# Performance work log

Hardware: AMD Instinct MI355X
Metric: run time of the kernel (lower is better)

## Reference

```python
import jax, jax.numpy as jnp
import numpy as np

N = 50000
E = 800000
F_IN = 512
HID = 32
HEADS = 8
CLS = 64
NEG_SLOPE = 0.2
EPS = 1e-16  # PyG softmax denominator epsilon


def setup_inputs() -> dict:
    key = jax.random.key(0)
    ks = jax.random.split(key, 10)
    x = jax.random.normal(ks[0], (N, F_IN), dtype=jnp.float32)
    edge_index = jax.random.randint(ks[1], (2, E), 0, N, dtype=jnp.int64)
    # layer 1: in=F_IN, heads=HEADS, out_per_head=HID, concat
    s1 = 1.0 / np.sqrt(F_IN)
    W1 = jax.random.normal(ks[2], (F_IN, HEADS * HID), dtype=jnp.float32) * s1
    att_src1 = jax.random.normal(ks[3], (HEADS, HID), dtype=jnp.float32) * 0.1
    att_dst1 = jax.random.normal(ks[4], (HEADS, HID), dtype=jnp.float32) * 0.1
    b1 = jnp.zeros((HEADS * HID,), dtype=jnp.float32)
    # layer 2: in=HEADS*HID, heads=1, out=CLS, no concat
    s2 = 1.0 / np.sqrt(HEADS * HID)
    W2 = jax.random.normal(ks[5], (HEADS * HID, CLS), dtype=jnp.float32) * s2
    att_src2 = jax.random.normal(ks[6], (1, CLS), dtype=jnp.float32) * 0.1
    att_dst2 = jax.random.normal(ks[7], (1, CLS), dtype=jnp.float32) * 0.1
    b2 = jnp.zeros((CLS,), dtype=jnp.float32)
    return {"x": x, "edge_index": edge_index,
            "W1": W1, "att_src1": att_src1, "att_dst1": att_dst1, "b1": b1,
            "W2": W2, "att_src2": att_src2, "att_dst2": att_dst2, "b2": b2}


def gat_conv(x, edge_index, W, att_src, att_dst, bias, concat):
    n = x.shape[0]
    heads, c = att_src.shape
    h = (x @ W).reshape(n, heads, c)                       # [N,H,C]
    # add self loops (PyG GATConv default)
    loop = jnp.arange(n, dtype=edge_index.dtype)
    src = jnp.concatenate([edge_index[0], loop])
    dst = jnp.concatenate([edge_index[1], loop])
    a_src = jnp.einsum('nhc,hc->nh', h, att_src)           # [N,H]
    a_dst = jnp.einsum('nhc,hc->nh', h, att_dst)
    e = a_src[src] + a_dst[dst]                            # [E',H]
    e = jax.nn.leaky_relu(e, NEG_SLOPE)
    # segment softmax over destination node
    m = jax.ops.segment_max(e, dst, num_segments=n)
    e = jnp.exp(e - jax.lax.stop_gradient(m)[dst])
    s = jax.ops.segment_sum(e, dst, num_segments=n)
    alpha = e / (s[dst] + EPS)                             # [E',H]
    msg = h[src] * alpha[:, :, None]                       # [E',H,C]
    out = jax.ops.segment_sum(msg, dst, num_segments=n)    # [N,H,C]
    out = out.reshape(n, heads * c) if concat else out.mean(axis=1)
    return out + bias


def reference(x, edge_index, W1, att_src1, att_dst1, b1, W2, att_src2, att_dst2, b2):
    h = gat_conv(x, edge_index, W1, att_src1, att_dst1, b1, concat=True)
    h = jax.nn.relu(h)
    # F.dropout with training=False (eval) is identity
    h = gat_conv(h, edge_index, W2, att_src2, att_dst2, b2, concat=False)
    return jax.nn.log_softmax(h, axis=1)
```

## Files before the change

kernel.cpp:

```cpp
#include <hip/hip_runtime.h>
#include <hip/hip_bf16.h>
#include <stdint.h>

#define F_IN 512
#define HID 32
#define HEADS 8
#define C1 (HEADS*HID)
#define CLS 64
#define NEG 0.2f
#define EPS 1e-16f

typedef __bf16 bf16x8 __attribute__((ext_vector_type(8)));
typedef __bf16 bf16x4 __attribute__((ext_vector_type(4)));
typedef float  f32x4  __attribute__((ext_vector_type(4)));

__device__ __forceinline__ float leaky(float v) { return v > 0.f ? v : NEG * v; }

__global__ __launch_bounds__(256) void cvt_x(const float* __restrict__ x,
    __bf16* __restrict__ xb, int total8) {
  int i = blockIdx.x * 256 + threadIdx.x;
  if (i >= total8) return;
  const float4* p = (const float4*)(x + (size_t)i * 8);
  float4 a = p[0], b = p[1];
  bf16x8 o;
  o[0] = (__bf16)a.x; o[1] = (__bf16)a.y; o[2] = (__bf16)a.z; o[3] = (__bf16)a.w;
  o[4] = (__bf16)b.x; o[5] = (__bf16)b.y; o[6] = (__bf16)b.z; o[7] = (__bf16)b.w;
  *(bf16x8*)(xb + (size_t)i * 8) = o;
}

__global__ __launch_bounds__(256) void cvt_w1t(const float* __restrict__ W1,
    __bf16* __restrict__ w1t) {
  int i = blockIdx.x * 256 + threadIdx.x;
  int o0 = i * 8;
  int c = o0 >> 9, k0 = o0 & 511;
  bf16x8 o;
#pragma unroll
  for (int j = 0; j < 8; j++) o[j] = (__bf16)W1[(size_t)(k0 + j) * C1 + c];
  *(bf16x8*)(w1t + (size_t)o0) = o;
}

__global__ __launch_bounds__(256) void cvt_w2t(const float* __restrict__ W2,
    __bf16* __restrict__ w2t) {
  int i = blockIdx.x * 256 + threadIdx.x;
  if (i >= CLS * C1 / 8) return;
  int o0 = i * 8;
  int c = o0 >> 8, k0 = o0 & 255;
  bf16x8 o;
#pragma unroll
  for (int j = 0; j < 8; j++) o[j] = (__bf16)W2[(size_t)(k0 + j) * CLS + c];
  *(bf16x8*)(w2t + (size_t)o0) = o;
}

__global__ __launch_bounds__(256) void gemm1_mfma(const __bf16* __restrict__ A,
    const __bf16* __restrict__ Bt, __bf16* __restrict__ C, int M) {
  __shared__ __bf16 Al[128 * 32];
  __shared__ __bf16 Bl[128 * 32];
  const int tid  = threadIdx.x;
  const int lane = tid & 63;
  const int wave = tid >> 6;
  const int lm = lane & 15, q = lane >> 4;
  const int wr = (wave >> 1) * 64, wc = (wave & 1) * 64;
  const int bm = blockIdx.y * 128, bn = blockIdx.x * 128;

  const int srow = tid >> 2;
  const int skc  = (tid & 3) * 8;

  f32x4 acc[4][4];
#pragma unroll
  for (int i = 0; i < 4; i++)
#pragma unroll
    for (int j = 0; j < 4; j++) acc[i][j] = (f32x4){0.f, 0.f, 0.f, 0.f};

  const int ra0 = min(bm + srow, M - 1);
  const int ra1 = min(bm + srow + 64, M - 1);
  const int rb0 = bn + srow, rb1 = bn + srow + 64;

  bf16x8 va0, va1, vb0, vb1;
  va0 = *(const bf16x8*)(A + (size_t)ra0 * 512 + skc);
  va1 = *(const bf16x8*)(A + (size_t)ra1 * 512 + skc);
  vb0 = *(const bf16x8*)(Bt + (size_t)rb0 * 512 + skc);
  vb1 = *(const bf16x8*)(Bt + (size_t)rb1 * 512 + skc);

  for (int kk = 0; kk < 16; kk++) {
    __syncthreads();
    *(bf16x8*)(Al + srow * 32 + skc)        = va0;
    *(bf16x8*)(Al + (srow + 64) * 32 + skc) = va1;
    *(bf16x8*)(Bl + srow * 32 + skc)        = vb0;
    *(bf16x8*)(Bl + (srow + 64) * 32 + skc) = vb1;
    __syncthreads();
    if (kk + 1 < 16) {
      const int k0 = (kk + 1) * 32;
      va0 = *(const bf16x8*)(A + (size_t)ra0 * 512 + k0 + skc);
      va1 = *(const bf16x8*)(A + (size_t)ra1 * 512 + k0 + skc);
      vb0 = *(const bf16x8*)(Bt + (size_t)rb0 * 512 + k0 + skc);
      vb1 = *(const bf16x8*)(Bt + (size_t)rb1 * 512 + k0 + skc);
    }
    bf16x8 af[4], bfr[4];
#pragma unroll
    for (int mi = 0; mi < 4; mi++)
      af[mi] = *(const bf16x8*)(Al + (wr + mi * 16 + lm) * 32 + q * 8);
#pragma unroll
    for (int ni = 0; ni < 4; ni++)
      bfr[ni] = *(const bf16x8*)(Bl + (wc + ni * 16 + lm) * 32 + q * 8);
#pragma unroll
    for (int mi = 0; mi < 4; mi++)
#pragma unroll
      for (int ni = 0; ni < 4; ni++)
        acc[mi][ni] = __builtin_amdgcn_mfma_f32_16x16x32_bf16(af[mi], bfr[ni], acc[mi][ni], 0, 0, 0);
  }

#pragma unroll
  for (int mi = 0; mi < 4; mi++) {
#pragma unroll
    for (int ni = 0; ni < 4; ni++) {
      const int col = bn + wc + ni * 16 + lm;
#pragma unroll
      for (int r = 0; r < 4; r++) {
        const int row = bm + wr + mi * 16 + q * 4 + r;
        if (row < M) C[(size_t)row * C1 + col] = (__bf16)acc[mi][ni][r];
      }
    }
  }
}

__global__ __launch_bounds__(256) void gemm2_mfma(const __bf16* __restrict__ A,
    const __bf16* __restrict__ Bt, __bf16* __restrict__ C, int M) {
  __shared__ __bf16 Al[128 * 32];
  __shared__ __bf16 Bl[64 * 32];
  const int tid  = threadIdx.x;
  const int lane = tid & 63;
  const int wave = tid >> 6;
  const int lm = lane & 15, q = lane >> 4;
  const int wr = (wave >> 1) * 64, wc = (wave & 1) * 32;
  const int bm = blockIdx.x * 128;

  const int srow = tid >> 2;
  const int skc  = (tid & 3) * 8;

  f32x4 acc[4][2];
#pragma unroll
  for (int i = 0; i < 4; i++)
#pragma unroll
    for (int j = 0; j < 2; j++) acc[i][j] = (f32x4){0.f, 0.f, 0.f, 0.f};

  const int ra0 = min(bm + srow, M - 1);
  const int ra1 = min(bm + srow + 64, M - 1);

  bf16x8 va0, va1, vb;
  va0 = *(const bf16x8*)(A + (size_t)ra0 * C1 + skc);
  va1 = *(const bf16x8*)(A + (size_t)ra1 * C1 + skc);
  vb  = *(const bf16x8*)(Bt + (size_t)srow * C1 + skc);

  for (int kk = 0; kk < 8; kk++) {
    __syncthreads();
    *(bf16x8*)(Al + srow * 32 + skc)        = va0;
    *(bf16x8*)(Al + (srow + 64) * 32 + skc) = va1;
    *(bf16x8*)(Bl + srow * 32 + skc)        = vb;
    __syncthreads();
    if (kk + 1 < 8) {
      const int k0 = (kk + 1) * 32;
      va0 = *(const bf16x8*)(A + (size_t)ra0 * C1 + k0 + skc);
      va1 = *(const bf16x8*)(A + (size_t)ra1 * C1 + k0 + skc);
      vb  = *(const bf16x8*)(Bt + (size_t)srow * C1 + k0 + skc);
    }
    bf16x8 af[4], bfr[2];
#pragma unroll
    for (int mi = 0; mi < 4; mi++)
      af[mi] = *(const bf16x8*)(Al + (wr + mi * 16 + lm) * 32 + q * 8);
#pragma unroll
    for (int ni = 0; ni < 2; ni++)
      bfr[ni] = *(const bf16x8*)(Bl + (wc + ni * 16 + lm) * 32 + q * 8);
#pragma unroll
    for (int mi = 0; mi < 4; mi++)
#pragma unroll
      for (int ni = 0; ni < 2; ni++)
        acc[mi][ni] = __builtin_amdgcn_mfma_f32_16x16x32_bf16(af[mi], bfr[ni], acc[mi][ni], 0, 0, 0);
  }

#pragma unroll
  for (int mi = 0; mi < 4; mi++) {
#pragma unroll
    for (int ni = 0; ni < 2; ni++) {
      const int col = wc + ni * 16 + lm;
#pragma unroll
      for (int r = 0; r < 4; r++) {
        const int row = bm + wr + mi * 16 + q * 4 + r;
        if (row < M) C[(size_t)row * CLS + col] = (__bf16)acc[mi][ni][r];
      }
    }
  }
}

__global__ __launch_bounds__(256) void att_scores1(const __bf16* __restrict__ h1,
    const float* __restrict__ asw, const float* __restrict__ adw,
    float* __restrict__ a_src, float* __restrict__ a_dst, int N) {
  const int t = threadIdx.x, lane = t & 63;
  const int n = blockIdx.x * 4 + (t >> 6);
  if (n >= N) return;
  bf16x4 x = *(const bf16x4*)(h1 + (size_t)n * C1 + lane * 4);
  const float4 wsv = *(const float4*)(asw + lane * 4);
  const float4 wdv = *(const float4*)(adw + lane * 4);
  float ps = (float)x[0] * wsv.x + (float)x[1] * wsv.y + (float)x[2] * wsv.z + (float)x[3] * wsv.w;
  float pd = (float)x[0] * wdv.x + (float)x[1] * wdv.y + (float)x[2] * wdv.z + (float)x[3] * wdv.w;
#pragma unroll
  for (int o = 1; o <= 4; o <<= 1) { ps += __shfl_xor(ps, o); pd += __shfl_xor(pd, o); }
  if ((lane & 7) == 0) {
    a_src[(size_t)n * 8 + (lane >> 3)] = ps;
    a_dst[(size_t)n * 8 + (lane >> 3)] = pd;
  }
}

__global__ __launch_bounds__(256) void att_scores2(const __bf16* __restrict__ h2b,
    const float* __restrict__ asw, const float* __restrict__ adw,
    float* __restrict__ a_src, float* __restrict__ a_dst, int N) {
  const int t = threadIdx.x, lane = t & 63;
  const int n = blockIdx.x * 4 + (t >> 6);
  if (n >= N) return;
  float v  = (float)h2b[(size_t)n * CLS + lane];
  float ps = v * asw[lane];
  float pd = v * adw[lane];
#pragma unroll
  for (int o = 1; o < 64; o <<= 1) { ps += __shfl_xor(ps, o); pd += __shfl_xor(pd, o); }
  if (lane == 0) { a_src[n] = ps; a_dst[n] = pd; }
}

__global__ __launch_bounds__(256) void count_deg(const int* __restrict__ ei,
    int* __restrict__ deg, int E) {
  int e = blockIdx.x * 256 + threadIdx.x;
  if (e < E) atomicAdd(&deg[ei[E + e]], 1);
}

__global__ __launch_bounds__(1024) void scan_rows(const int* __restrict__ deg,
    int* __restrict__ rowstart, int N) {
  __shared__ int wpart[16];
  __shared__ int s_carry;
  const int t = threadIdx.x, lane = t & 63, wid = t >> 6;
  if (t == 0) s_carry = 0;
  __syncthreads();
  for (int base = 0; base < N; base += 8192) {
    int i0 = base + t * 8;
    int d0[8], s8 = 0;
#pragma unroll
    for (int k = 0; k < 8; k++) { int i = i0 + k; d0[k] = (i < N) ? deg[i] : 0; s8 += d0[k]; }
    int v = s8;
#pragma unroll
    for (int off = 1; off < 64; off <<= 1) { int x = __shfl_up(v, off); if (lane >= off) v += x; }
    if (lane == 63) wpart[wid] = v;
    __syncthreads();
    if (wid == 0) {
      int w = (lane < 16) ? wpart[lane] : 0;
#pragma unroll
      for (int off = 1; off < 16; off <<= 1) { int x = __shfl_up(w, off); if (lane >= off) w += x; }
      if (lane < 16) wpart[lane] = w;
    }
    __syncthreads();
    int excl = s_carry + (wid > 0 ? wpart[wid - 1] : 0) + v - s8;
#pragma unroll
    for (int k = 0; k < 8; k++) { int i = i0 + k; if (i < N) rowstart[i] = excl; excl += d0[k]; }
    __syncthreads();
    if (t == 0) s_carry += wpart[15];
    __syncthreads();
  }
  if (t == 0) rowstart[N] = s_carry;
}

__global__ __launch_bounds__(256) void scatter_csr(const int* __restrict__ ei,
    int* __restrict__ cur, int* __restrict__ csr_src, int E) {
  int e = blockIdx.x * 256 + threadIdx.x;
  if (e >= E) return;
  int s = ei[e], d = ei[E + e];
  int pos = atomicAdd(&cur[d], 1);
  csr_src[pos] = s;
}

__global__ __launch_bounds__(256) void gather1(const int* __restrict__ rowstart,
    const int* __restrict__ csr_src, const __bf16* __restrict__ h1,
    const float* __restrict__ as1, const float* __restrict__ ad1,
    const float* __restrict__ b1, __bf16* __restrict__ o1, int N) {
  const int t = threadIdx.x;
  const int d = blockIdx.x * 4 + (t >> 6);
  if (d >= N) return;
  const int lane = t & 63;
  const int e8 = lane >> 3, hh = lane & 7;
  const int r0 = rowstart[d];
  const int deg = rowstart[d + 1] - r0;

  const float addh = ad1[(size_t)d * 8 + hh];
  const float self_sc = leaky(as1[(size_t)d * 8 + hh] + addh);

  int   se[8];
  float sc[8];
#pragma unroll
  for (int ch = 0; ch < 8; ch++) {
    const int j = ch * 8 + e8;
    se[ch] = 0; sc[ch] = -3.4e38f;
    if (j < deg) {
      int s = csr_src[r0 + j];
      se[ch] = s;
      sc[ch] = leaky(as1[(size_t)s * 8 + hh] + addh);
    }
  }
  float mx = -3.4e38f;
#pragma unroll
  for (int ch = 0; ch < 8; ch++) mx = fmaxf(mx, sc[ch]);
  for (int j0 = 64; j0 < deg; j0 += 8) {
    int j = j0 + e8;
    if (j < deg) {
      int s = csr_src[r0 + j];
      mx = fmaxf(mx, leaky(as1[(size_t)s * 8 + hh] + addh));
    }
  }
  mx = fmaxf(mx, __shfl_xor(mx, 8));
  mx = fmaxf(mx, __shfl_xor(mx, 16));
  mx = fmaxf(mx, __shfl_xor(mx, 32));
  mx = fmaxf(mx, self_sc);

  float sum = 0.f;
#pragma unroll
  for (int ch = 0; ch < 8; ch++)
    if (ch * 8 + e8 < deg) sum += __expf(sc[ch] - mx);
  for (int j0 = 64; j0 < deg; j0 += 8) {
    int j = j0 + e8;
    if (j < deg) {
      int s = csr_src[r0 + j];
      sum += __expf(leaky(as1[(size_t)s * 8 + hh] + addh) - mx);
    }
  }
  sum += __shfl_xor(sum, 8);
  sum += __shfl_xor(sum, 16);
  sum += __shfl_xor(sum, 32);
  sum += __expf(self_sc - mx);
  const float inv = 1.f / (sum + EPS);

  float al[8];
#pragma unroll
  for (int ch = 0; ch < 8; ch++) al[ch] = __expf(sc[ch] - mx) * inv;
  const float al_self_byhh = __expf(self_sc - mx) * inv;

  const int p = lane >> 5, g = lane & 31, hg = g >> 2;
  float acc[8];
#pragma unroll
  for (int i = 0; i < 8; i++) acc[i] = 0.f;

#pragma unroll
  for (int it = 0; it < 32; it++) {
    if (it * 2 < deg) {
      const int   j   = it * 2 + p;
      const int   s_j = __shfl(se[it >> 2], (j & 7) * 8);
      const float a_j = __shfl(al[it >> 2], (j & 7) * 8 + hg);
      bf16x8 x = *(const bf16x8*)(h1 + (size_t)s_j * C1 + g * 8);
#pragma unroll
      for (int i = 0; i < 8; i++) acc[i] += a_j * (float)x[i];
    }
  }
  for (int j0 = 64; j0 < deg; j0 += 8) {
    int j = j0 + e8;
    int se2 = 0; float al2 = 0.f;
    if (j < deg) { se2 = csr_src[r0 + j]; al2 = __expf(leaky(as1[(size_t)se2 * 8 + hh] + addh) - mx) * inv; }
#pragma unroll
    for (int it = 0; it < 4; it++) {
      if (j0 + it * 2 < deg) {
        const int   jj  = it * 2 + p;
        const int   s_j = __shfl(se2, jj * 8);
        const float a_j = __shfl(al2, jj * 8 + hg);
        bf16x8 x = *(const bf16x8*)(h1 + (size_t)s_j * C1 + g * 8);
#pragma unroll
        for (int i = 0; i < 8; i++) acc[i] += a_j * (float)x[i];
      }
    }
  }
#pragma unroll
  for (int i = 0; i < 8; i++) acc[i] += __shfl_xor(acc[i], 32);

  const float a_selfh = __shfl(al_self_byhh, hg);
  if (lane < 32) {
    bf16x8 xs = *(const bf16x8*)(h1 + (size_t)d * C1 + g * 8);
    const float4 b4a = *(const float4*)(b1 + g * 8);
    const float4 b4b = *(const float4*)(b1 + g * 8 + 4);
    bf16x8 o;
    o[0] = (__bf16)fmaxf(acc[0] + a_selfh * (float)xs[0] + b4a.x, 0.f);
    o[1] = (__bf16)fmaxf(acc[1] + a_selfh * (float)xs[1] + b4a.y, 0.f);
    o[2] = (__bf16)fmaxf(acc[2] + a_selfh * (float)xs[2] + b4a.z, 0.f);
    o[3] = (__bf16)fmaxf(acc[3] + a_selfh * (float)xs[3] + b4a.w, 0.f);
    o[4] = (__bf16)fmaxf(acc[4] + a_selfh * (float)xs[4] + b4b.x, 0.f);
    o[5] = (__bf16)fmaxf(acc[5] + a_selfh * (float)xs[5] + b4b.y, 0.f);
    o[6] = (__bf16)fmaxf(acc[6] + a_selfh * (float)xs[6] + b4b.z, 0.f);
    o[7] = (__bf16)fmaxf(acc[7] + a_selfh * (float)xs[7] + b4b.w, 0.f);
    *(bf16x8*)(o1 + (size_t)d * C1 + g * 8) = o;
  }
}

__global__ __launch_bounds__(256) void gather2(const int* __restrict__ rowstart,
    const int* __restrict__ csr_src, const __bf16* __restrict__ h2b,
    const float* __restrict__ as2, const float* __restrict__ ad2,
    float* __restrict__ out, int N) {
  const int t = threadIdx.x, lane = t & 63;
  const int d = blockIdx.x * 4 + (t >> 6);
  if (d >= N) return;
  const int r0 = rowstart[d], deg = rowstart[d + 1] - r0;
  const float addd = ad2[d];
  const float self_sc = leaky(as2[d] + addd);

  int se = 0; float sc = -3.4e38f;
  if (lane < deg) { se = csr_src[r0 + lane]; sc = leaky(as2[se] + addd); }
  float mx = sc;
  for (int j0 = 64; j0 < deg; j0 += 64) {
    int j = j0 + lane;
    if (j < deg) mx = fmaxf(mx, leaky(as2[csr_src[r0 + j]] + addd));
  }
#pragma unroll
  for (int o = 1; o < 64; o <<= 1) mx = fmaxf(mx, __shfl_xor(mx, o));
  mx = fmaxf(mx, self_sc);

  float ex = (lane < deg) ? __expf(sc - mx) : 0.f;
  float sum = ex;
  for (int j0 = 64; j0 < deg; j0 += 64) {
    int j = j0 + lane;
    if (j < deg) sum += __expf(leaky(as2[csr_src[r0 + j]] + addd) - mx);
  }
#pragma unroll
  for (int o = 1; o < 64; o <<= 1) sum += __shfl_xor(sum, o);
  const float e_self = __expf(self_sc - mx);
  sum += e_self;
  const float inv = 1.f / (sum + EPS);
  const float alpha = ex * inv;
  const float al_self = e_self * inv;

  const int e8 = lane >> 3, c8 = lane & 7;
  float acc[8];
#pragma unroll
  for (int i = 0; i < 8; i++) acc[i] = 0.f;

#pragma unroll
  for (int it = 0; it < 8; it++) {
    if (it * 8 < deg) {
      const int   j   = it * 8 + e8;
      const int   s_j = __shfl(se, j);
      const float a_j = __shfl(alpha, j);
      bf16x8 x = *(const bf16x8*)(h2b + (size_t)s_j * CLS + c8 * 8);
#pragma unroll
      for (int i = 0; i < 8; i++) acc[i] += a_j * (float)x[i];
    }
  }
  for (int j0 = 64; j0 < deg; j0 += 64) {
    int j = j0 + lane;
    int se2 = 0; float al2 = 0.f;
    if (j < deg) { se2 = csr_src[r0 + j]; al2 = __expf(leaky(as2[se2] + addd) - mx) * inv; }
#pragma unroll
    for (int it = 0; it < 8; it++) {
      if (j0 + it * 8 < deg) {
        const int   jj  = it * 8 + e8;
        const int   s_j = __shfl(se2, jj);
        const float a_j = __shfl(al2, jj);
        bf16x8 x = *(const bf16x8*)(h2b + (size_t)s_j * CLS + c8 * 8);
#pragma unroll
        for (int i = 0; i < 8; i++) acc[i] += a_j * (float)x[i];
      }
    }
  }
#pragma unroll
  for (int i = 0; i < 8; i++) {
    acc[i] += __shfl_xor(acc[i], 8);
    acc[i] += __shfl_xor(acc[i], 16);
    acc[i] += __shfl_xor(acc[i], 32);
  }
  if (lane < 8) {
    bf16x8 xs = *(const bf16x8*)(h2b + (size_t)d * CLS + c8 * 8);
    float4 o0, o1v;
    o0.x  = acc[0] + al_self * (float)xs[0];
    o0.y  = acc[1] + al_self * (float)xs[1];
    o0.z  = acc[2] + al_self * (float)xs[2];
    o0.w  = acc[3] + al_self * (float)xs[3];
    o1v.x = acc[4] + al_self * (float)xs[4];
    o1v.y = acc[5] + al_self * (float)xs[5];
    o1v.z = acc[6] + al_self * (float)xs[6];
    o1v.w = acc[7] + al_self * (float)xs[7];
    *(float4*)(out + (size_t)d * CLS + c8 * 8)     = o0;
    *(float4*)(out + (size_t)d * CLS + c8 * 8 + 4) = o1v;
  }
}

__global__ __launch_bounds__(256) void final_lsm(float* __restrict__ out,
    const float* __restrict__ b2, int N) {
  const int t = threadIdx.x, c = t & 63;
  const int n = blockIdx.x * 4 + (t >> 6);
  if (n >= N) return;
  float v = out[(size_t)n * CLS + c] + b2[c];
  float mx = v;
#pragma unroll
  for (int o = 1; o < 64; o <<= 1) mx = fmaxf(mx, __shfl_xor(mx, o));
  float ex = __expf(v - mx);
  float sm = ex;
#pragma unroll
  for (int o = 1; o < 64; o <<= 1) sm += __shfl_xor(sm, o);
  out[(size_t)n * CLS + c] = v - mx - __logf(sm);
}

extern "C" void kernel_launch(void* const* d_in, const int* in_sizes, int n_in,
                              void* d_out, int out_size, void* d_ws, size_t ws_size,
                              hipStream_t stream) {
  const float* x        = (const float*)d_in[0];
  const int*   ei       = (const int*)d_in[1];
  const float* W1       = (const float*)d_in[2];
  const float* att_src1 = (const float*)d_in[3];
  const float* att_dst1 = (const float*)d_in[4];
  const float* b1       = (const float*)d_in[5];
  const float* W2       = (const float*)d_in[6];
  const float* att_src2 = (const float*)d_in[7];
  const float* att_dst2 = (const float*)d_in[8];
  const float* b2       = (const float*)d_in[9];
  float* out = (float*)d_out;

  const int N  = in_sizes[0] / F_IN;
  const int E  = in_sizes[1] / 2;

  char* ws = (char*)d_ws;
  size_t off = 0;
  auto alloc = [&](size_t bytes) -> void* {
    void* p = ws + off;
    off += (bytes + 255) & ~(size_t)255;
    return p;
  };
  __bf16* h1  = (__bf16*)alloc((size_t)N * C1 * 2);
  __bf16* o1  = (__bf16*)alloc((size_t)N * C1 * 2);
  float*  as1 = (float*)alloc((size_t)N * HEADS * 4);
  float*  ad1 = (float*)alloc((size_t)N * HEADS * 4);
  __bf16* h2b = (__bf16*)alloc((size_t)N * CLS * 2);
  float*  as2 = (float*)alloc((size_t)N * 4);
  float*  ad2 = (float*)alloc((size_t)N * 4);
  int* deg      = (int*)alloc((size_t)N * 4);
  int* rowstart = (int*)alloc((size_t)(N + 1) * 4);
  int* cur      = (int*)alloc((size_t)N * 4);
  int* csr_src  = (int*)alloc((size_t)E * 4);
  __bf16* xb  = (__bf16*)alloc((size_t)N * F_IN * 2);
  __bf16* w1t = (__bf16*)alloc((size_t)C1 * F_IN * 2);
  __bf16* w2t = (__bf16*)alloc((size_t)CLS * C1 * 2);

  cvt_x<<<(N * F_IN / 8 + 255) / 256, 256, 0, stream>>>(x, xb, N * F_IN / 8);
  cvt_w1t<<<(C1 * F_IN / 8 + 255) / 256, 256, 0, stream>>>(W1, w1t);
  cvt_w2t<<<(CLS * C1 / 8 + 255) / 256, 256, 0, stream>>>(W2, w2t);

  hipMemsetAsync(deg, 0, (size_t)N * 4, stream);
  count_deg<<<(E + 255) / 256, 256, 0, stream>>>(ei, deg, E);
  scan_rows<<<1, 1024, 0, stream>>>(deg, rowstart, N);
  hipMemcpyAsync(cur, rowstart, (size_t)N * 4, hipMemcpyDeviceToDevice, stream);
  scatter_csr<<<(E + 255) / 256, 256, 0, stream>>>(ei, cur, csr_src, E);

  {
    dim3 g(C1 / 128, (N + 127) / 128);
    gemm1_mfma<<<g, 256, 0, stream>>>(xb, w1t, h1, N);
  }
  att_scores1<<<(N + 3) / 4, 256, 0, stream>>>(h1, att_src1, att_dst1, as1, ad1, N);
  gather1<<<(N + 3) / 4, 256, 0, stream>>>(rowstart, csr_src, h1, as1, ad1, b1, o1, N);

  gemm2_mfma<<<(N + 127) / 128, 256, 0, stream>>>(o1, w2t, h2b, N);
  att_scores2<<<(N + 3) / 4, 256, 0, stream>>>(h2b, att_src2, att_dst2, as2, ad2, N);
  gather2<<<(N + 3) / 4, 256, 0, stream>>>(rowstart, csr_src, h2b, as2, ad2, out, N);

  final_lsm<<<(N + 3) / 4, 256, 0, stream>>>(out, b2, N);
}
```

Baseline: 481.5 us.

## Fuse x conversion into GEMM, merge prep kernels, parallel scan, fuse log-softmax

The fp32 to bf16 conversion of x now happens inside the first GEMM's load path, which removes a separate pass that read x and wrote a bf16 copy. The weight transposes and degree counting are merged into one prep kernel. The single-block row scan is replaced with a three-kernel multi-block scan that also fills the cursor array, so the device-to-device copy goes away. The bias add and log-softmax are folded into gather2, removing the final_lsm pass over the output. In exchange, gemm1 now reads fp32 A tiles, doubling the bytes it loads for A, and more small kernels are launched for the scan.

```diff
diff --git a/kernel.cpp b/kernel.cpp
--- a/kernel.cpp
+++ b/kernel.cpp
@@ -16,42 +16,106 @@
 
 __device__ __forceinline__ float leaky(float v) { return v > 0.f ? v : NEG * v; }
 
-__global__ __launch_bounds__(256) void cvt_x(const float* __restrict__ x,
-    __bf16* __restrict__ xb, int total8) {
-  int i = blockIdx.x * 256 + threadIdx.x;
-  if (i >= total8) return;
-  const float4* p = (const float4*)(x + (size_t)i * 8);
-  float4 a = p[0], b = p[1];
+__device__ __forceinline__ bf16x8 cvt8(float4 a, float4 b) {
   bf16x8 o;
   o[0] = (__bf16)a.x; o[1] = (__bf16)a.y; o[2] = (__bf16)a.z; o[3] = (__bf16)a.w;
   o[4] = (__bf16)b.x; o[5] = (__bf16)b.y; o[6] = (__bf16)b.z; o[7] = (__bf16)b.w;
-  *(bf16x8*)(xb + (size_t)i * 8) = o;
-}
-
-__global__ __launch_bounds__(256) void cvt_w1t(const float* __restrict__ W1,
-    __bf16* __restrict__ w1t) {
-  int i = blockIdx.x * 256 + threadIdx.x;
-  int o0 = i * 8;
-  int c = o0 >> 9, k0 = o0 & 511;
-  bf16x8 o;
-#pragma unroll
-  for (int j = 0; j < 8; j++) o[j] = (__bf16)W1[(size_t)(k0 + j) * C1 + c];
-  *(bf16x8*)(w1t + (size_t)o0) = o;
-}
-
-__global__ __launch_bounds__(256) void cvt_w2t(const float* __restrict__ W2,
-    __bf16* __restrict__ w2t) {
-  int i = blockIdx.x * 256 + threadIdx.x;
-  if (i >= CLS * C1 / 8) return;
-  int o0 = i * 8;
-  int c = o0 >> 8, k0 = o0 & 255;
-  bf16x8 o;
-#pragma unroll
-  for (int j = 0; j < 8; j++) o[j] = (__bf16)W2[(size_t)(k0 + j) * CLS + c];
-  *(bf16x8*)(w2t + (size_t)o0) = o;
-}
-
-__global__ __launch_bounds__(256) void gemm1_mfma(const __bf16* __restrict__ A,
+  return o;
+}
+
+__global__ __launch_bounds__(256) void prep(const float* __restrict__ W1,
+    const float* __restrict__ W2, const int* __restrict__ ei,
+    __bf16* __restrict__ w1t, __bf16* __restrict__ w2t,
+    int* __restrict__ deg, int E) {
+  const int b = blockIdx.x, t = threadIdx.x;
+  if (b < 64) {
+    int i = b * 256 + t;
+    int o0 = i * 8;
+    int c = o0 >> 9, k0 = o0 & 511;
+    bf16x8 o;
+#pragma unroll
+    for (int j = 0; j < 8; j++) o[j] = (__bf16)W1[(size_t)(k0 + j) * C1 + c];
+    *(bf16x8*)(w1t + (size_t)o0) = o;
+  } else if (b < 72) {
+    int i = (b - 64) * 256 + t;
+    int o0 = i * 8;
+    int c = o0 >> 8, k0 = o0 & 255;
+    bf16x8 o;
+#pragma unroll
+    for (int j = 0; j < 8; j++) o[j] = (__bf16)W2[(size_t)(k0 + j) * CLS + c];
+    *(bf16x8*)(w2t + (size_t)o0) = o;
+  } else {
+    int e = (b - 72) * 256 + t;
+    if (e < E) atomicAdd(&deg[ei[E + e]], 1);
+  }
+}
+
+__global__ __launch_bounds__(256) void scan_k1(const int* __restrict__ deg,
+    int* __restrict__ bsum, int N) {
+  __shared__ int ws[4];
+  const int t = threadIdx.x, lane = t & 63, wid = t >> 6;
+  int i = blockIdx.x * 256 + t;
+  int v = (i < N) ? deg[i] : 0;
+#pragma unroll
+  for (int o = 1; o < 64; o <<= 1) v += __shfl_xor(v, o);
+  if (lane == 0) ws[wid] = v;
+  __syncthreads();
+  if (t == 0) bsum[blockIdx.x] = ws[0] + ws[1] + ws[2] + ws[3];
+}
+
+__global__ __launch_bounds__(256) void scan_k2(int* __restrict__ bsum, int nb) {
+  __shared__ int wsum[4];
+  __shared__ int carry_s;
+  const int t = threadIdx.x, lane = t & 63, wid = t >> 6;
+  if (t == 0) carry_s = 0;
+  __syncthreads();
+  for (int base = 0; base < nb; base += 256) {
+    int i = base + t;
+    int v = (i < nb) ? bsum[i] : 0;
+    int inc = v;
+#pragma unroll
+    for (int o = 1; o < 64; o <<= 1) { int x = __shfl_up(inc, o); if (lane >= o) inc += x; }
+    if (lane == 63) wsum[wid] = inc;
+    __syncthreads();
+    int woff = 0;
+    for (int w = 0; w < wid; w++) woff += wsum[w];
+    int excl = carry_s + woff + inc - v;
+    if (i < nb) bsum[i] = excl;
+    __syncthreads();
+    if (t == 0) carry_s += wsum[0] + wsum[1] + wsum[2] + wsum[3];
+    __syncthreads();
+  }
+}
+
+__global__ __launch_bounds__(256) void scan_k3(const int* __restrict__ deg,
+    const int* __restrict__ bsum, int* __restrict__ rowstart,
+    int* __restrict__ cur, int N) {
+  __shared__ int wsum[4];
+  const int t = threadIdx.x, lane = t & 63, wid = t >> 6;
+  int i = blockIdx.x * 256 + t;
+  int v = (i < N) ? deg[i] : 0;
+  int inc = v;
+#pragma unroll
+  for (int o = 1; o < 64; o <<= 1) { int x = __shfl_up(inc, o); if (lane >= o) inc += x; }
+  if (lane == 63) wsum[wid] = inc;
+  __syncthreads();
+  int woff = 0;
+  for (int w = 0; w < wid; w++) woff += wsum[w];
+  int excl = bsum[blockIdx.x] + woff + inc - v;
+  if (i < N) { rowstart[i] = excl; cur[i] = excl; }
+  if (i == N - 1) rowstart[N] = excl + v;
+}
+
+__global__ __launch_bounds__(256) void scatter_csr(const int* __restrict__ ei,
+    int* __restrict__ cur, int* __restrict__ csr_src, int E) {
+  int e = blockIdx.x * 256 + threadIdx.x;
+  if (e >= E) return;
+  int s = ei[e], d = ei[E + e];
+  int pos = atomicAdd(&cur[d], 1);
+  csr_src[pos] = s;
+}
+
+__global__ __launch_bounds__(256) void gemm1_mfma(const float* __restrict__ A,
     const __bf16* __restrict__ Bt, __bf16* __restrict__ C, int M) {
   __shared__ __bf16 Al[128 * 32];
   __shared__ __bf16 Bl[128 * 32];
@@ -75,23 +139,28 @@
   const int ra1 = min(bm + srow + 64, M - 1);
   const int rb0 = bn + srow, rb1 = bn + srow + 64;
 
-  bf16x8 va0, va1, vb0, vb1;
-  va0 = *(const bf16x8*)(A + (size_t)ra0 * 512 + skc);
-  va1 = *(const bf16x8*)(A + (size_t)ra1 * 512 + skc);
+  float4 a0x, a0y, a1x, a1y;
+  bf16x8 vb0, vb1;
+  a0x = *(const float4*)(A + (size_t)ra0 * 512 + skc);
+  a0y = *(const float4*)(A + (size_t)ra0 * 512 + skc + 4);
+  a1x = *(const float4*)(A + (size_t)ra1 * 512 + skc);
+  a1y = *(const float4*)(A + (size_t)ra1 * 512 + skc + 4);
   vb0 = *(const bf16x8*)(Bt + (size_t)rb0 * 512 + skc);
   vb1 = *(const bf16x8*)(Bt + (size_t)rb1 * 512 + skc);
 
   for (int kk = 0; kk < 16; kk++) {
     __syncthreads();
-    *(bf16x8*)(Al + srow * 32 + skc)        = va0;
-    *(bf16x8*)(Al + (srow + 64) * 32 + skc) = va1;
+    *(bf16x8*)(Al + srow * 32 + skc)        = cvt8(a0x, a0y);
+    *(bf16x8*)(Al + (srow + 64) * 32 + skc) = cvt8(a1x, a1y);
     *(bf16x8*)(Bl + srow * 32 + skc)        = vb0;
     *(bf16x8*)(Bl + (srow + 64) * 32 + skc) = vb1;
     __syncthreads();
     if (kk + 1 < 16) {
       const int k0 = (kk + 1) * 32;
-      va0 = *(const bf16x8*)(A + (size_t)ra0 * 512 + k0 + skc);
-      va1 = *(const bf16x8*)(A + (size_t)ra1 * 512 + k0 + skc);
+      a0x = *(const float4*)(A + (size_t)ra0 * 512 + k0 + skc);
+      a0y = *(const float4*)(A + (size_t)ra0 * 512 + k0 + skc + 4);
+      a1x = *(const float4*)(A + (size_t)ra1 * 512 + k0 + skc);
+      a1y = *(const float4*)(A + (size_t)ra1 * 512 + k0 + skc + 4);
       vb0 = *(const bf16x8*)(Bt + (size_t)rb0 * 512 + k0 + skc);
       vb1 = *(const bf16x8*)(Bt + (size_t)rb1 * 512 + k0 + skc);
     }
@@ -222,55 +291,6 @@
 #pragma unroll
   for (int o = 1; o < 64; o <<= 1) { ps += __shfl_xor(ps, o); pd += __shfl_xor(pd, o); }
   if (lane == 0) { a_src[n] = ps; a_dst[n] = pd; }
-}
-
-__global__ __launch_bounds__(256) void count_deg(const int* __restrict__ ei,
-    int* __restrict__ deg, int E) {
-  int e = blockIdx.x * 256 + threadIdx.x;
-  if (e < E) atomicAdd(&deg[ei[E + e]], 1);
-}
-
-__global__ __launch_bounds__(1024) void scan_rows(const int* __restrict__ deg,
-    int* __restrict__ rowstart, int N) {
-  __shared__ int wpart[16];
-  __shared__ int s_carry;
-  const int t = threadIdx.x, lane = t & 63, wid = t >> 6;
-  if (t == 0) s_carry = 0;
-  __syncthreads();
-  for (int base = 0; base < N; base += 8192) {
-    int i0 = base + t * 8;
-    int d0[8], s8 = 0;
-#pragma unroll
-    for (int k = 0; k < 8; k++) { int i = i0 + k; d0[k] = (i < N) ? deg[i] : 0; s8 += d0[k]; }
-    int v = s8;
-#pragma unroll
-    for (int off = 1; off < 64; off <<= 1) { int x = __shfl_up(v, off); if (lane >= off) v += x; }
-    if (lane == 63) wpart[wid] = v;
-    __syncthreads();
-    if (wid == 0) {
-      int w = (lane < 16) ? wpart[lane] : 0;
-#pragma unroll
-      for (int off = 1; off < 16; off <<= 1) { int x = __shfl_up(w, off); if (lane >= off) w += x; }
-      if (lane < 16) wpart[lane] = w;
-    }
-    __syncthreads();
-    int excl = s_carry + (wid > 0 ? wpart[wid - 1] : 0) + v - s8;
-#pragma unroll
-    for (int k = 0; k < 8; k++) { int i = i0 + k; if (i < N) rowstart[i] = excl; excl += d0[k]; }
-    __syncthreads();
-    if (t == 0) s_carry += wpart[15];
-    __syncthreads();
-  }
-  if (t == 0) rowstart[N] = s_carry;
-}
-
-__global__ __launch_bounds__(256) void scatter_csr(const int* __restrict__ ei,
-    int* __restrict__ cur, int* __restrict__ csr_src, int E) {
-  int e = blockIdx.x * 256 + threadIdx.x;
-  if (e >= E) return;
-  int s = ei[e], d = ei[E + e];
-  int pos = atomicAdd(&cur[d], 1);
-  csr_src[pos] = s;
 }
 
 __global__ __launch_bounds__(256) void gather1(const int* __restrict__ rowstart,
@@ -393,7 +413,7 @@
 __global__ __launch_bounds__(256) void gather2(const int* __restrict__ rowstart,
     const int* __restrict__ csr_src, const __bf16* __restrict__ h2b,
     const float* __restrict__ as2, const float* __restrict__ ad2,
-    float* __restrict__ out, int N) {
+    const float* __restrict__ b2, float* __restrict__ out, int N) {
   const int t = threadIdx.x, lane = t & 63;
   const int d = blockIdx.x * 4 + (t >> 6);
   if (d >= N) return;
@@ -464,36 +484,39 @@
     acc[i] += __shfl_xor(acc[i], 16);
     acc[i] += __shfl_xor(acc[i], 32);
   }
+
+  bf16x8 xs = *(const bf16x8*)(h2b + (size_t)d * CLS + c8 * 8);
+  const float4 bba = *(const float4*)(b2 + c8 * 8);
+  const float4 bbb = *(const float4*)(b2 + c8 * 8 + 4);
+  float v[8];
+  v[0] = acc[0] + al_self * (float)xs[0] + bba.x;
+  v[1] = acc[1] + al_self * (float)xs[1] + bba.y;
+  v[2] = acc[2] + al_self * (float)xs[2] + bba.z;
+  v[3] = acc[3] + al_self * (float)xs[3] + bba.w;
+  v[4] = acc[4] + al_self * (float)xs[4] + bbb.x;
+  v[5] = acc[5] + al_self * (float)xs[5] + bbb.y;
+  v[6] = acc[6] + al_self * (float)xs[6] + bbb.z;
+  v[7] = acc[7] + al_self * (float)xs[7] + bbb.w;
+  float m2 = v[0];
+#pragma unroll
+  for (int i = 1; i < 8; i++) m2 = fmaxf(m2, v[i]);
+  m2 = fmaxf(m2, __shfl_xor(m2, 1));
+  m2 = fmaxf(m2, __shfl_xor(m2, 2));
+  m2 = fmaxf(m2, __shfl_xor(m2, 4));
+  float sm = 0.f;
+#pragma unroll
+  for (int i = 0; i < 8; i++) sm += __expf(v[i] - m2);
+  sm += __shfl_xor(sm, 1);
+  sm += __shfl_xor(sm, 2);
+  sm += __shfl_xor(sm, 4);
+  const float lg = m2 + __logf(sm);
   if (lane < 8) {
-    bf16x8 xs = *(const bf16x8*)(h2b + (size_t)d * CLS + c8 * 8);
     float4 o0, o1v;
-    o0.x  = acc[0] + al_self * (float)xs[0];
-    o0.y  = acc[1] + al_self * (float)xs[1];
-    o0.z  = acc[2] + al_self * (float)xs[2];
-    o0.w  = acc[3] + al_self * (float)xs[3];
-    o1v.x = acc[4] + al_self * (float)xs[4];
-    o1v.y = acc[5] + al_self * (float)xs[5];
-    o1v.z = acc[6] + al_self * (float)xs[6];
-    o1v.w = acc[7] + al_self * (float)xs[7];
+    o0.x  = v[0] - lg; o0.y  = v[1] - lg; o0.z  = v[2] - lg; o0.w  = v[3] - lg;
+    o1v.x = v[4] - lg; o1v.y = v[5] - lg; o1v.z = v[6] - lg; o1v.w = v[7] - lg;
     *(float4*)(out + (size_t)d * CLS + c8 * 8)     = o0;
     *(float4*)(out + (size_t)d * CLS + c8 * 8 + 4) = o1v;
   }
-}
-
-__global__ __launch_bounds__(256) void final_lsm(float* __restrict__ out,
-    const float* __restrict__ b2, int N) {
-  const int t = threadIdx.x, c = t & 63;
-  const int n = blockIdx.x * 4 + (t >> 6);
-  if (n >= N) return;
-  float v = out[(size_t)n * CLS + c] + b2[c];
-  float mx = v;
-#pragma unroll
-  for (int o = 1; o < 64; o <<= 1) mx = fmaxf(mx, __shfl_xor(mx, o));
-  float ex = __expf(v - mx);
-  float sm = ex;
-#pragma unroll
-  for (int o = 1; o < 64; o <<= 1) sm += __shfl_xor(sm, o);
-  out[(size_t)n * CLS + c] = v - mx - __logf(sm);
 }
 
 extern "C" void kernel_launch(void* const* d_in, const int* in_sizes, int n_in,
@@ -513,6 +536,7 @@
 
   const int N  = in_sizes[0] / F_IN;
   const int E  = in_sizes[1] / 2;
+  const int NB = (N + 255) / 256;
 
   char* ws = (char*)d_ws;
   size_t off = 0;
@@ -532,30 +556,26 @@
   int* rowstart = (int*)alloc((size_t)(N + 1) * 4);
   int* cur      = (int*)alloc((size_t)N * 4);
   int* csr_src  = (int*)alloc((size_t)E * 4);
-  __bf16* xb  = (__bf16*)alloc((size_t)N * F_IN * 2);
+  int* bsum     = (int*)alloc((size_t)NB * 4);
   __bf16* w1t = (__bf16*)alloc((size_t)C1 * F_IN * 2);
   __bf16* w2t = (__bf16*)alloc((size_t)CLS * C1 * 2);
 
-  cvt_x<<<(N * F_IN / 8 + 255) / 256, 256, 0, stream>>>(x, xb, N * F_IN / 8);
-  cvt_w1t<<<(C1 * F_IN / 8 + 255) / 256, 256, 0, stream>>>(W1, w1t);
-  cvt_w2t<<<(CLS * C1 / 8 + 255) / 256, 256, 0, stream>>>(W2, w2t);
-
   hipMemsetAsync(deg, 0, (size_t)N * 4, stream);
-  count_deg<<<(E + 255) / 256, 256, 0, stream>>>(ei, deg, E);
-  scan_rows<<<1, 1024, 0, stream>>>(deg, rowstart, N);
-  hipMemcpyAsync(cur, rowstart, (size_t)N * 4, hipMemcpyDeviceToDevice, stream);
+  prep<<<72 + (E + 255) / 256, 256, 0, stream>>>(W1, W2, ei, w1t, w2t, deg, E);
+
+  scan_k1<<<NB, 256, 0, stream>>>(deg, bsum, N);
+  scan_k2<<<1, 256, 0, stream>>>(bsum, NB);
+  scan_k3<<<NB, 256, 0, stream>>>(deg, bsum, rowstart, cur, N);
   scatter_csr<<<(E + 255) / 256, 256, 0, stream>>>(ei, cur, csr_src, E);
 
   {
     dim3 g(C1 / 128, (N + 127) / 128);
-    gemm1_mfma<<<g, 256, 0, stream>>>(xb, w1t, h1, N);
+    gemm1_mfma<<<g, 256, 0, stream>>>(x, w1t, h1, N);
   }
   att_scores1<<<(N + 3) / 4, 256, 0, stream>>>(h1, att_src1, att_dst1, as1, ad1, N);
   gather1<<<(N + 3) / 4, 256, 0, stream>>>(rowstart, csr_src, h1, as1, ad1, b1, o1, N);
 
   gemm2_mfma<<<(N + 127) / 128, 256, 0, stream>>>(o1, w2t, h2b, N);
   att_scores2<<<(N + 3) / 4, 256, 0, stream>>>(h2b, att_src2, att_dst2, as2, ad2, N);
-  gather2<<<(N + 3) / 4, 256, 0, stream>>>(rowstart, csr_src, h2b, as2, ad2, out, N);
-
-  final_lsm<<<(N + 3) / 4, 256, 0, stream>>>(out, b2, N);
-}
+  gather2<<<(N + 3) / 4, 256, 0, stream>>>(rowstart, csr_src, h2b, as2, ad2, b2, out, N);
+}
```

Result: faster. 414.9 us (-13.8%).
